# Optimization experiments

Hardware: AMD Instinct MI355X
Metric: run time of the kernel (lower is better)

## Reference

```python
import jax, jax.numpy as jnp
import numpy as np
from functools import partial

NP = 1024      # particles
T = 128        # timesteps
CUR_MIN, CUR_MAX = -2.0, 4.0
E_CRIT = 29000.0
F_STD = 0.005
G_STD = 0.01
NU = 1.0 / (G_STD * np.sqrt(2.0 * np.pi))

# VoC battery open-circuit-voltage curve constants
V_L, V_0 = -1.59614486, 4.13646328
GAMMA, ALPHA, BETA = 0.63726463, 1.40174122, 2.54478965


def voc(soc):
    return (V_L + (V_0 - V_L) * jnp.exp(GAMMA * (soc - 1.0))
            + ALPHA * V_L * (soc - 1.0)
            + (1.0 - ALPHA) * V_L * (jnp.exp(-BETA) - jnp.exp(-BETA * jnp.sqrt(soc))))


def setup_inputs() -> dict:
    key = jax.random.key(0)
    ks = jax.random.split(key, 11)
    soc_init = jax.random.uniform(ks[0], (NP, 1), jnp.float32, 0.3, 1.0)
    current = jax.random.normal(ks[1], (1, T), jnp.float32) * 0.5 + 1.0
    voltage_measured = 3.7 + 0.1 * jax.random.normal(ks[2], (1, T), jnp.float32)
    W1 = jax.random.normal(ks[3], (2, 1024), jnp.float32) / np.sqrt(2.0)
    b1 = jnp.zeros((1024,), jnp.float32)
    W2 = jax.random.normal(ks[4], (1024, 512), jnp.float32) / np.sqrt(1024.0)
    b2 = jnp.zeros((512,), jnp.float32)
    W3 = jax.random.normal(ks[5], (512, 1), jnp.float32) / np.sqrt(512.0)
    b3 = jnp.zeros((1,), jnp.float32)
    noise = jax.random.normal(ks[6], (T, NP, 1), jnp.float32)  # unit-std process noise
    u = jax.random.uniform(ks[7], (T,), jnp.float32)           # systematic-resampling offsets
    return {"soc_init": soc_init, "current": current, "voltage_measured": voltage_measured,
            "W1": W1, "b1": b1, "W2": W2, "b2": b2, "W3": W3, "b3": b3,
            "noise": noise, "u": u}


def _forward(soc_init, current, voltage_measured, W1, b1, W2, b2, W3, b3, noise, u):
    n = soc_init.shape[0]

    def mlp(x):  # [n,2] -> [n,1]
        z = jax.nn.sigmoid(x @ W1 + b1)
        z = jax.nn.sigmoid(z @ W2 + b2)
        return z @ W3 + b3

    def scale_I(I):
        return (I - CUR_MIN) / (CUR_MAX - CUR_MIN)

    cur = current[0]                       # [T]
    vmeas = voltage_measured[0]            # [T]
    cur_prev = jnp.concatenate([cur[:1], cur[:-1]])  # first step reuses current[0,0]

    def step(soc, xs):
        c_prev, c_t, vm, eps, ut = xs
        # --- prediction with previous current ---
        I = jnp.broadcast_to(c_prev, soc.shape)
        Z = mlp(jnp.concatenate([soc, scale_I(I)], axis=1))
        V = voc(soc) - I * Z
        soc = soc - I * V / E_CRIT + eps * F_STD
        soc = jnp.clip(soc, 1e-10, 1.0)
        # --- measurement update with current at t ---
        I = jnp.broadcast_to(c_t, soc.shape)
        sI = scale_I(I)
        Z = mlp(jnp.concatenate([soc, sI], axis=1))
        V = voc(soc) - I * Z
        logW = np.log(NU) - 0.5 * ((V - vm) / G_STD) ** 2  # [n,1]
        w = jnp.exp(logW - jnp.max(logW))[:, 0]
        wn = w / jnp.sum(w)
        # systematic resampling (deterministic given offset ut)
        cdf = jnp.cumsum(wn)
        pos = (ut + jnp.arange(n, dtype=jnp.float32)) / n
        idx = jnp.clip(jnp.searchsorted(cdf, pos), 0, n - 1)
        soc = soc[idx]
        # --- post-resample evaluation ---
        Z = mlp(jnp.concatenate([soc, sI], axis=1))
        V = voc(soc) - I * Z
        mse = jnp.mean((V - vm) ** 2)
        return soc, (mse, V[:, 0], soc[:, 0])

    soc0 = soc_init.astype(jnp.float32)
    _, (mses, Vs, socs) = jax.lax.scan(step, soc0, (cur_prev, cur, vmeas, noise, u))
    loss = jnp.mean(mses)        # == sum_t mse_t / T
    voltage = Vs.T               # [n, T]
    soc_hist = socs.T            # [n, T]
    return loss, voltage, soc_hist


def reference(soc_init, current, voltage_measured, W1, b1, W2, b2, W3, b3, noise, u):
    return _forward(soc_init, current, voltage_measured, W1, b1, W2, b2, W3, b3, noise, u)
```

## Files before the change

kernel.cpp:

```cpp
#include <hip/hip_runtime.h>
#include <stdint.h>

typedef __attribute__((ext_vector_type(8))) short short8;
typedef __attribute__((ext_vector_type(4))) float floatx4;

#define DONE_MAGIC 0x600DF00Du


__device__ __forceinline__ float sigm(float x) { return 1.0f / (1.0f + expf(-x)); }

__device__ __forceinline__ float vocf(float s) {
  const float V_L = -1.59614486f, V_0 = 4.13646328f;
  const float GAM = 0.63726463f, ALP = 1.40174122f, BET = 2.54478965f;
  return V_L + (V_0 - V_L) * expf(GAM * (s - 1.0f)) + ALP * V_L * (s - 1.0f)
       + (1.0f - ALP) * V_L * (expf(-BET) - expf(-BET * sqrtf(s)));
}

__device__ __forceinline__ unsigned short f2bf(float f) {
  unsigned u = __float_as_uint(f);
  u += 0x7FFFu + ((u >> 16) & 1u);
  return (unsigned short)(u >> 16);
}
__device__ __forceinline__ float bf2f(unsigned short b) {
  return __uint_as_float(((unsigned)b) << 16);
}

__device__ __forceinline__ float interp_c(const float* ctab, float s) {
  float f = s * 31.0f;
  float jf = fminf(floorf(f), 30.0f);
  int j = (int)jf;
  float u = f - jf;
  const float4 c = *(const float4*)&ctab[j * 4];
  return fmaf(fmaf(fmaf(c.w, u, c.z), u, c.y), u, c.x);
}

__device__ __forceinline__ int send_bl(float c, float u) {
  float C = c * 1024.0f;
  float sf = floorf(C - u);
  sf += (u + (sf + 1.0f) <= C) ? 1.0f : 0.0f;
  sf -= (u + sf > C) ? 1.0f : 0.0f;
  return (int)sf;
}

__device__ __forceinline__ float fast_exp2(float x) {
  float r;
  asm("v_exp_f32 %0, %1" : "=v"(r) : "v"(x));
  return r;
}


template<int C, int RM>
__device__ __forceinline__ float dpp_add_f(float x) {
  return __int_as_float(__builtin_amdgcn_update_dpp(0, __float_as_int(x), C, RM, 0xF, false));
}
template<int C, int RM>
__device__ __forceinline__ float dpp_old_f(float x) {
  return __int_as_float(__builtin_amdgcn_update_dpp(__float_as_int(x), __float_as_int(x), C, RM, 0xF, false));
}
template<int C, int RM>
__device__ __forceinline__ int dpp_old_i(int x) {
  return __builtin_amdgcn_update_dpp(x, x, C, RM, 0xF, false);
}
__device__ __forceinline__ float dpp_wshr1_f0(float x) {
  return __int_as_float(__builtin_amdgcn_update_dpp(0, __float_as_int(x), 0x138, 0xF, 0xF, true));
}
__device__ __forceinline__ int dpp_wshr1_i(int x, int old) {
  return __builtin_amdgcn_update_dpp(old, x, 0x138, 0xF, 0xF, false);
}
__device__ __forceinline__ int dpp_wshl1_i(int x, int old) {
  return __builtin_amdgcn_update_dpp(old, x, 0x130, 0xF, 0xF, false);
}

__device__ __forceinline__ float wave_iscan_add(float x) {
  x += dpp_add_f<0x111, 0xF>(x);
  x += dpp_add_f<0x112, 0xF>(x);
  x += dpp_add_f<0x114, 0xF>(x);
  x += dpp_add_f<0x118, 0xF>(x);
  x += dpp_add_f<0x142, 0xA>(x);
  x += dpp_add_f<0x143, 0xC>(x);
  return x;
}
__device__ __forceinline__ float wave_max_l63(float x) {
  x = fmaxf(x, dpp_old_f<0xB1,  0xF>(x));
  x = fmaxf(x, dpp_old_f<0x4E,  0xF>(x));
  x = fmaxf(x, dpp_old_f<0x141, 0xF>(x));
  x = fmaxf(x, dpp_old_f<0x140, 0xF>(x));
  x = fmaxf(x, dpp_old_f<0x142, 0xA>(x));
  x = fmaxf(x, dpp_old_f<0x143, 0xC>(x));
  return x;
}
__device__ __forceinline__ int wave_iscan_max(int x) {
  x = max(x, dpp_old_i<0x111, 0xF>(x));
  x = max(x, dpp_old_i<0x112, 0xF>(x));
  x = max(x, dpp_old_i<0x114, 0xF>(x));
  x = max(x, dpp_old_i<0x118, 0xF>(x));
  x = max(x, dpp_old_i<0x142, 0xA>(x));
  x = max(x, dpp_old_i<0x143, 0xC>(x));
  return x;
}

__device__ __forceinline__ float rdlane_f(float x, int lane) {
  return __int_as_float(__builtin_amdgcn_readlane(__float_as_int(x), lane));
}

__device__ __forceinline__ void bar_lds() {
  asm volatile("s_waitcnt lgkmcnt(0)" ::: "memory");
  __builtin_amdgcn_s_barrier();
  asm volatile("" ::: "memory");
}


__global__ void __launch_bounds__(256)
k1_swizzle(const float* __restrict__ W2g, short* __restrict__ w2hiG, short* __restrict__ w2loG)
{
  int bid = blockIdx.x, tid = threadIdx.x;
  int pg = bid & 15, ng = bid >> 4;
  int u = pg * 256 + tid;
  int kb = u >> 7, l = u & 63, nt = (u >> 6) & 1, kq = l >> 4;
  int col = ng * 32 + nt * 16 + (l & 15);
  short8 hi8, lo8;
  #pragma unroll
  for (int j = 0; j < 8; j++) {
    int k = kb * 32 + kq * 8 + j;
    float w = W2g[k * 512 + col];
    unsigned short h = f2bf(w);
    hi8[j] = (short)h;
    lo8[j] = (short)f2bf(w - bf2f(h));
  }
  size_t off = ((size_t)ng * 4096 + u) * 8;
  *(short8*)(w2hiG + off) = hi8;
  *(short8*)(w2loG + off) = lo8;
}


__global__ void __launch_bounds__(256)
k2_gemm(const float* __restrict__ curg, const float* __restrict__ W1g,
        const float* __restrict__ b1g, const float* __restrict__ b2g,
        const float* __restrict__ W3g, const short* __restrict__ w2hiG,
        const short* __restrict__ w2loG, float* __restrict__ part)
{
  __shared__ short w2S[32768];
  __shared__ float b2S[32], w3S[32];

  const int tid = threadIdx.x, bid = blockIdx.x;
  const int ng = bid & 15, rtg = bid >> 4;
  const int wv = tid >> 6, ln = tid & 63;
  const int kq = ln >> 4;

  {
    const short* srcH = w2hiG + (size_t)ng * 32768;
    for (int i = tid; i < 4096; i += 256)
      *(short8*)(w2S + i * 8) = *(const short8*)(srcH + i * 8);
    if (tid < 32) { b2S[tid] = b2g[ng * 32 + tid]; w3S[tid] = W3g[ng * 32 + tid]; }
  }
  __syncthreads();

  const short* loG = w2loG + (size_t)ng * 32768;
  const int c = ln & 15, q = ln >> 4;
  const float b20 = b2S[c], b21 = b2S[16 + c];
  const float w30 = w3S[c], w31 = w3S[16 + c];

  for (int jj = 0; jj < 3; jj++) {
    int rt = rtg + 32 * jj;
    if (rt >= 72) break;
    int pt = rt * 4 + wv;
    unsigned r = pt * 16 + (ln & 15);
    unsigned t = r / 36u;
    int i = (int)(r - t * 36u);
    float soc = (float)(i - 1) * (1.0f / 31.0f);
    float sI = (curg[t] + 2.0f) / 6.0f;

    floatx4 acc0 = {0.f, 0.f, 0.f, 0.f};
    floatx4 acc1 = {0.f, 0.f, 0.f, 0.f};

    for (int kb = 0; kb < 32; kb++) {
      int k0 = kb * 32 + kq * 8;
      floatx4 wa0 = *(const floatx4*)(W1g + k0);
      floatx4 wa1 = *(const floatx4*)(W1g + k0 + 4);
      floatx4 wb0 = *(const floatx4*)(W1g + 1024 + k0);
      floatx4 wb1 = *(const floatx4*)(W1g + 1024 + k0 + 4);
      floatx4 bb0 = *(const floatx4*)(b1g + k0);
      floatx4 bb1 = *(const floatx4*)(b1g + k0 + 4);
      short8 ah, al;
      #pragma unroll
      for (int j = 0; j < 4; j++) {
        float x = soc * wa0[j] + sI * wb0[j] + bb0[j];
        float z = __builtin_amdgcn_rcpf(1.0f + __expf(-x));
        unsigned short h = f2bf(z);
        ah[j] = (short)h;
        al[j] = (short)f2bf(z - bf2f(h));
      }
      #pragma unroll
      for (int j = 0; j < 4; j++) {
        float x = soc * wa1[j] + sI * wb1[j] + bb1[j];
        float z = __builtin_amdgcn_rcpf(1.0f + __expf(-x));
        unsigned short h = f2bf(z);
        ah[4 + j] = (short)h;
        al[4 + j] = (short)f2bf(z - bf2f(h));
      }
      short8 bh0 = *(const short8*)(w2S + (kb * 2 + 0) * 512 + ln * 8);
      short8 bh1 = *(const short8*)(w2S + (kb * 2 + 1) * 512 + ln * 8);
      short8 bl0 = *(const short8*)(loG + (kb * 2 + 0) * 512 + ln * 8);
      short8 bl1 = *(const short8*)(loG + (kb * 2 + 1) * 512 + ln * 8);
      acc0 = __builtin_amdgcn_mfma_f32_16x16x32_bf16(ah, bh0, acc0, 0, 0, 0);
      acc1 = __builtin_amdgcn_mfma_f32_16x16x32_bf16(ah, bh1, acc1, 0, 0, 0);
      acc0 = __builtin_amdgcn_mfma_f32_16x16x32_bf16(ah, bl0, acc0, 0, 0, 0);
      acc1 = __builtin_amdgcn_mfma_f32_16x16x32_bf16(ah, bl1, acc1, 0, 0, 0);
      acc0 = __builtin_amdgcn_mfma_f32_16x16x32_bf16(al, bh0, acc0, 0, 0, 0);
      acc1 = __builtin_amdgcn_mfma_f32_16x16x32_bf16(al, bh1, acc1, 0, 0, 0);
    }

    #pragma unroll
    for (int r2 = 0; r2 < 4; r2++) {
      float v = w30 * sigm(acc0[r2] + b20) + w31 * sigm(acc1[r2] + b21);
      v += __shfl_xor(v, 1);
      v += __shfl_xor(v, 2);
      v += __shfl_xor(v, 4);
      v += __shfl_xor(v, 8);
      if (c == 0) part[(size_t)(pt * 16 + q * 4 + r2) * 16 + ng] = v;
    }
  }
}


__global__ void __launch_bounds__(256)
k3_table(const float* __restrict__ part, const float* __restrict__ b3g,
         const float* __restrict__ curg, float* __restrict__ VtabG)
{
  unsigned r = blockIdx.x * 256 + threadIdx.x;
  if (r < 4608) {
    const float* p = part + (size_t)r * 16;
    float s = 0.f;
    #pragma unroll
    for (int i = 0; i < 16; i++) s += p[i];
    float Z = s + b3g[0];
    unsigned t = r / 36u;
    int i = (int)(r - t * 36u);
    float node = (float)(i - 1) * (1.0f / 31.0f);
    float nodc = fmaxf(node, 1e-10f);
    VtabG[r] = vocf(nodc) - curg[t] * Z;
  }
}


__global__ void __launch_bounds__(256)
k3b_coeff(const float* __restrict__ VtabG, float* __restrict__ ctabG)
{
  int idx = blockIdx.x * 256 + threadIdx.x;
  if (idx < 3968) {
    int t = idx / 31, j = idx - t * 31;
    const float* nb = VtabG + t * 36 + j;
    float n0 = nb[0], n1 = nb[1], n2 = nb[2], n3 = nb[3];
    float c0 = n1;
    float c1 = (-2.0f * n0 - 3.0f * n1 + 6.0f * n2 - n3) * (1.0f / 6.0f);
    float c2 = (n0 - 2.0f * n1 + n2) * 0.5f;
    float c3 = (-n0 + 3.0f * (n1 - n2) + n3) * (1.0f / 6.0f);
    *(float4*)&ctabG[idx * 4] = make_float4(c0, c1, c2, c3);
  }
}


__device__ __forceinline__ int swzi(int j) { return ((j & 3) << 8) | (j >> 2); }

__global__ void __launch_bounds__(256)
pf_seq(const float* __restrict__ soc_init, const float* __restrict__ curg,
       const float* __restrict__ vmeasg, const float* __restrict__ noise_g,
       const float* __restrict__ u_g, const float* __restrict__ ctabG,
       float* __restrict__ vout, float* __restrict__ sout, float* __restrict__ outp,
       unsigned* __restrict__ flag)
{
  __shared__ float ctabS[15872];
  __shared__ float2 pvS[2][1024];
  __shared__ int   markS[1024] __attribute__((aligned(16)));
  __shared__ float maxS[4], sumS[4], lossS[4];
  __shared__ int   seFS[4], tagS[4];

  if (blockIdx.x != 0) {
    float a = 1.0000001f, b = 0.9999999f, c = 0.5f;
    while (__hip_atomic_load(flag, __ATOMIC_RELAXED, __HIP_MEMORY_SCOPE_AGENT) != DONE_MAGIC) {
      #pragma unroll 8
      for (int i = 0; i < 512; i++) { a = fmaf(a, c, b); b = fmaf(b, c, a); }
    }
    asm volatile("" :: "v"(a), "v"(b));
    return;
  }

  const int tid = threadIdx.x;
  const int w = tid >> 6, l = tid & 63;
  const int p0 = tid * 4;

  #pragma unroll
  for (int k = 0; k < 16; k++) {
    int i = tid + 256 * k;
    if (i < 3968) *(float4*)&ctabS[i * 4] = *(const float4*)&ctabG[i * 4];
  }
  float curA = curg[l],   curB = curg[64 + l];
  float vmA  = vmeasg[l], vmB  = vmeasg[64 + l];
  float uA   = u_g[l],    uB   = u_g[64 + l];
  *(int4*)&markS[p0] = make_int4(-1, -1, -1, -1);

  float sp[4];
  {
    float4 s4 = *(const float4*)(soc_init + p0);
    float4 n4 = *(const float4*)(noise_g + p0);
    bar_lds();
    float c0 = rdlane_f(curA, 0);
    float c02 = c0 * (1.0f / 29000.0f);
    #pragma unroll
    for (int r = 0; r < 4; r++) {
      float si = ((const float*)&s4)[r];
      float V0 = interp_c(ctabS, si);
      float spn = fmaf(((const float*)&n4)[r], 0.005f, fmaf(-c02, V0, si));
      sp[r] = __builtin_amdgcn_fmed3f(spn, 1e-10f, 1.0f);
    }
  }

  float lossAcc = 0.0f;

  for (int t = 0; t < 128; t++) {
    const float* ctab = ctabS + t * 124;
    const int cb = t & 1;
    float cI, vm, ut;
    if (t < 64) { cI = rdlane_f(curA, t); vm = rdlane_f(vmA, t); ut = rdlane_f(uA, t); }
    else        { cI = rdlane_f(curB, t - 64); vm = rdlane_f(vmB, t - 64); ut = rdlane_f(uB, t - 64); }
    float cI2 = cI * (1.0f / 29000.0f);

    int tn = (t < 127) ? t + 1 : 127;
    float4 noi4 = *(const float4*)(noise_g + tn * 1024 + p0);

    float lw[4];
    #pragma unroll
    for (int r = 0; r < 4; r++) {
      float V1 = interp_c(ctab, sp[r]);
      pvS[cb][r * 256 + tid] = make_float2(sp[r], V1);
      float dd = V1 - vm;
      lw[r] = dd * dd * -7213.4755594f;
    }

    float lmax = fmaxf(fmaxf(lw[0], lw[1]), fmaxf(lw[2], lw[3]));
    float wm = wave_max_l63(lmax);
    if (l == 63) maxS[w] = wm;
    bar_lds();
    float m = fmaxf(fmaxf(maxS[0], maxS[1]), fmaxf(maxS[2], maxS[3]));

    float pr[4], acc = 0.0f;
    #pragma unroll
    for (int r = 0; r < 4; r++) { float wr = fast_exp2(lw[r] - m); acc += wr; pr[r] = acc; }
    float isc = wave_iscan_add(acc);
    if (l == 63) sumS[w] = isc;
    bar_lds();
    float s0 = sumS[0], s1 = sumS[1], s2 = sumS[2], s3 = sumS[3];
    float total = (s0 + s1) + (s2 + s3);
    float woff = (w > 0 ? s0 : 0.0f) + (w > 1 ? s1 : 0.0f) + (w > 2 ? s2 : 0.0f);
    float excl = dpp_wshr1_f0(isc) + woff;
    float rS = 1.0f / total;

    int se[4];
    #pragma unroll
    for (int r = 0; r < 4; r++) se[r] = send_bl((excl + pr[r]) * rS, ut);
    if (l == 0) seFS[w] = se[0];
    bar_lds();
    int nf = 0;
    if (w < 3) nf = seFS[w + 1];
    int nxt = dpp_wshl1_i(se[0], nf);
    int tbase = t << 10;
    if (tid == 0 && se[0] >= 0) markS[0] = tbase;
    #pragma unroll
    for (int r = 0; r < 4; r++) {
      int j = p0 + r;
      int slot = se[r] + 1;
      if (j == 1023) {
        if (slot <= 1023) markS[swzi(slot)] = tbase | 1023;
      } else {
        int seN = (r < 3) ? se[r + 1] : nxt;
        if (seN > se[r] && slot <= 1023) markS[swzi(slot)] = tbase | (j + 1);
      }
    }
    bar_lds();

    int mk0 = markS[tid],       mk1 = markS[256 + tid];
    int mk2 = markS[512 + tid], mk3 = markS[768 + tid];
    int q0 = mk0;
    int q1 = max(q0, mk1);
    int q2 = max(q1, mk2);
    int q3 = max(q2, mk3);
    int iscI = wave_iscan_max(q3);
    if (l == 63) tagS[w] = iscI;
    bar_lds();
    int ex = dpp_wshr1_i(iscI, -1);
    if (w > 0) ex = max(ex, tagS[0]);
    if (w > 1) ex = max(ex, tagS[1]);
    if (w > 2) ex = max(ex, tagS[2]);

    int o0 = max(ex, q0) & 1023, o1 = max(ex, q1) & 1023;
    int o2 = max(ex, q2) & 1023, o3 = max(ex, q3) & 1023;
    float2 g0 = pvS[cb][swzi(o0)];
    float2 g1 = pvS[cb][swzi(o1)];
    float2 g2 = pvS[cb][swzi(o2)];
    float2 g3 = pvS[cb][swzi(o3)];

    *(float4*)(vout + t * 1024 + p0) = make_float4(g0.y, g1.y, g2.y, g3.y);
    *(float4*)(sout + t * 1024 + p0) = make_float4(g0.x, g1.x, g2.x, g3.x);

    float2 g[4] = {g0, g1, g2, g3};
    #pragma unroll
    for (int r = 0; r < 4; r++) {
      float d = g[r].y - vm;
      lossAcc = fmaf(d, d, lossAcc);
      float spn = fmaf(((const float*)&noi4)[r], 0.005f, fmaf(-cI2, g[r].y, g[r].x));
      sp[r] = __builtin_amdgcn_fmed3f(spn, 1e-10f, 1.0f);
    }
  }

  float ls = wave_iscan_add(lossAcc);
  if (l == 63) lossS[w] = ls;
  bar_lds();
  if (tid == 0) {
    outp[0] = (lossS[0] + lossS[1] + lossS[2] + lossS[3]) * (1.0f / 131072.0f);
    __hip_atomic_store(flag, DONE_MAGIC, __ATOMIC_RELEASE, __HIP_MEMORY_SCOPE_AGENT);
  }
}


__global__ void __launch_bounds__(256)
k5_transpose(const float* __restrict__ vout, const float* __restrict__ sout,
             float* __restrict__ outp)
{
  __shared__ float tile[128 * 65];
  const int bid = blockIdx.x;
  const int arr = bid & 1;
  const int pg = bid >> 1;
  const float* src = arr ? sout : vout;
  float* dst = outp + 1 + arr * 131072;
  const int tid = threadIdx.x;
  const int p0 = pg * 64;

  #pragma unroll 4
  for (int s = 0; s < 32; s++) {
    int t = s * 4 + (tid >> 6);
    int p = tid & 63;
    tile[t * 65 + p] = src[t * 1024 + p0 + p];
  }
  __syncthreads();
  #pragma unroll 4
  for (int s = 0; s < 32; s++) {
    int pl = s * 2 + (tid >> 7);
    int t = tid & 127;
    dst[(p0 + pl) * 128 + t] = tile[t * 65 + pl];
  }
}


extern "C" void kernel_launch(void* const* d_in, const int* in_sizes, int n_in,
                              void* d_out, int out_size, void* d_ws, size_t ws_size,
                              hipStream_t stream) {
  const float* soc_init = (const float*)d_in[0];
  const float* cur      = (const float*)d_in[1];
  const float* vmeas    = (const float*)d_in[2];
  const float* W1       = (const float*)d_in[3];
  const float* b1       = (const float*)d_in[4];
  const float* W2       = (const float*)d_in[5];
  const float* b2       = (const float*)d_in[6];
  const float* W3       = (const float*)d_in[7];
  const float* b3       = (const float*)d_in[8];
  const float* noise    = (const float*)d_in[9];
  const float* u        = (const float*)d_in[10];
  float* out = (float*)d_out;
  char* ws = (char*)d_ws;

  short* w2hi   = (short*)ws;
  short* w2lo   = (short*)(ws + (1 << 20));
  float* part   = (float*)(ws + (2 << 20));
  char*  p3     = ws + (2 << 20) + 4608 * 16 * 4;
  float* VtabG  = (float*)p3;
  float* ctabG  = (float*)(p3 + 4608 * 4);
  float* vout   = (float*)(p3 + 4608 * 4 + 3968 * 16);
  float* sout   = (float*)(p3 + 4608 * 4 + 3968 * 16 + 1024 * 128 * 4);
  unsigned* flag = (unsigned*)(p3 + 4608 * 4 + 3968 * 16 + 2 * 1024 * 128 * 4);

  k1_swizzle<<<256, 256, 0, stream>>>(W2, w2hi, w2lo);
  k2_gemm<<<512, 256, 0, stream>>>(cur, W1, b1, b2, W3, w2hi, w2lo, part);
  k3_table<<<18, 256, 0, stream>>>(part, b3, cur, VtabG);
  k3b_coeff<<<16, 256, 0, stream>>>(VtabG, ctabG);
  pf_seq<<<256, 256, 0, stream>>>(soc_init, cur, vmeas, noise, u, ctabG, vout, sout, out, flag);
  k5_transpose<<<32, 256, 0, stream>>>(vout, sout, out);
}
```

Measured before the change: 342.6 us.

## Cut per-step block barriers by merging max/sum pass and using chunk atomics

Merges the max-reduction and sum-scan barriers into one: each wave uses its own local max for the exponentials and publishes a (max, sum) pair, and the cross-wave offsets are rescaled by exp2 factors afterwards. The boundary barrier for the next wave's first search result goes away, since the neighbour value is taken from lane data. The tag-scan barrier is replaced by LDS atomicMax into per-chunk maxima during marking. This removes about three block barriers per timestep in a single-block serial loop, at the cost of LDS atomics and slightly different floating-point rounding in the normalised CDF. There is also a redundant f3 computation left in.

```diff
diff --git a/kernel.cpp b/kernel.cpp
--- a/kernel.cpp
+++ b/kernel.cpp
@@ -80,14 +80,14 @@
   x += dpp_add_f<0x143, 0xC>(x);
   return x;
 }
-__device__ __forceinline__ float wave_max_l63(float x) {
+__device__ __forceinline__ float wave_max_bcast(float x) {
   x = fmaxf(x, dpp_old_f<0xB1,  0xF>(x));
   x = fmaxf(x, dpp_old_f<0x4E,  0xF>(x));
   x = fmaxf(x, dpp_old_f<0x141, 0xF>(x));
   x = fmaxf(x, dpp_old_f<0x140, 0xF>(x));
   x = fmaxf(x, dpp_old_f<0x142, 0xA>(x));
   x = fmaxf(x, dpp_old_f<0x143, 0xC>(x));
-  return x;
+  return __int_as_float(__builtin_amdgcn_readlane(__float_as_int(x), 63));
 }
 __device__ __forceinline__ int wave_iscan_max(int x) {
   x = max(x, dpp_old_i<0x111, 0xF>(x));
@@ -272,8 +272,9 @@
   __shared__ float ctabS[15872];
   __shared__ float2 pvS[2][1024];
   __shared__ int   markS[1024] __attribute__((aligned(16)));
-  __shared__ float maxS[4], sumS[4], lossS[4];
-  __shared__ int   seFS[4], tagS[4];
+  __shared__ int   chunkS[4] __attribute__((aligned(16)));
+  __shared__ float2 msS[4] __attribute__((aligned(16)));
+  __shared__ float lossS[4];
 
   if (blockIdx.x != 0) {
     float a = 1.0000001f, b = 0.9999999f, c = 0.5f;
@@ -298,21 +299,24 @@
   float vmA  = vmeasg[l], vmB  = vmeasg[64 + l];
   float uA   = u_g[l],    uB   = u_g[64 + l];
   *(int4*)&markS[p0] = make_int4(-1, -1, -1, -1);
-
-  float sp[4];
+  if (tid < 4) chunkS[tid] = -1;
+
+  float sp0, sp1, sp2, sp3;
   {
     float4 s4 = *(const float4*)(soc_init + p0);
     float4 n4 = *(const float4*)(noise_g + p0);
     bar_lds();
     float c0 = rdlane_f(curA, 0);
     float c02 = c0 * (1.0f / 29000.0f);
+    float spv[4];
     #pragma unroll
     for (int r = 0; r < 4; r++) {
       float si = ((const float*)&s4)[r];
       float V0 = interp_c(ctabS, si);
       float spn = fmaf(((const float*)&n4)[r], 0.005f, fmaf(-c02, V0, si));
-      sp[r] = __builtin_amdgcn_fmed3f(spn, 1e-10f, 1.0f);
-    }
+      spv[r] = __builtin_amdgcn_fmed3f(spn, 1e-10f, 1.0f);
+    }
+    sp0 = spv[0]; sp1 = spv[1]; sp2 = spv[2]; sp3 = spv[3];
   }
 
   float lossAcc = 0.0f;
@@ -328,69 +332,92 @@
     int tn = (t < 127) ? t + 1 : 127;
     float4 noi4 = *(const float4*)(noise_g + tn * 1024 + p0);
 
-    float lw[4];
-    #pragma unroll
-    for (int r = 0; r < 4; r++) {
-      float V1 = interp_c(ctab, sp[r]);
-      pvS[cb][r * 256 + tid] = make_float2(sp[r], V1);
-      float dd = V1 - vm;
-      lw[r] = dd * dd * -7213.4755594f;
-    }
-
-    float lmax = fmaxf(fmaxf(lw[0], lw[1]), fmaxf(lw[2], lw[3]));
-    float wm = wave_max_l63(lmax);
-    if (l == 63) maxS[w] = wm;
+    float V10 = interp_c(ctab, sp0);
+    float V11 = interp_c(ctab, sp1);
+    float V12 = interp_c(ctab, sp2);
+    float V13 = interp_c(ctab, sp3);
+    pvS[cb][tid]       = make_float2(sp0, V10);
+    pvS[cb][256 + tid] = make_float2(sp1, V11);
+    pvS[cb][512 + tid] = make_float2(sp2, V12);
+    pvS[cb][768 + tid] = make_float2(sp3, V13);
+    float d0 = V10 - vm, d1 = V11 - vm, d2 = V12 - vm, d3 = V13 - vm;
+    float lw0 = d0 * d0 * -7213.4755594f;
+    float lw1 = d1 * d1 * -7213.4755594f;
+    float lw2 = d2 * d2 * -7213.4755594f;
+    float lw3 = d3 * d3 * -7213.4755594f;
+
+    float lmax = fmaxf(fmaxf(lw0, lw1), fmaxf(lw2, lw3));
+    float mw = wave_max_bcast(lmax);
+    float pr0, pr1, pr2, pr3, acc;
+    {
+      float w0 = fast_exp2(lw0 - mw); acc = w0;    pr0 = acc;
+      float w1 = fast_exp2(lw1 - mw); acc += w1;   pr1 = acc;
+      float w2 = fast_exp2(lw2 - mw); acc += w2;   pr2 = acc;
+      float w3 = fast_exp2(lw3 - mw); acc += w3;   pr3 = acc;
+    }
+    float isc = wave_iscan_add(acc);
+    if (l == 63) msS[w] = make_float2(mw, isc);
     bar_lds();
-    float m = fmaxf(fmaxf(maxS[0], maxS[1]), fmaxf(maxS[2], maxS[3]));
-
-    float pr[4], acc = 0.0f;
-    #pragma unroll
-    for (int r = 0; r < 4; r++) { float wr = fast_exp2(lw[r] - m); acc += wr; pr[r] = acc; }
-    float isc = wave_iscan_add(acc);
-    if (l == 63) sumS[w] = isc;
-    bar_lds();
-    float s0 = sumS[0], s1 = sumS[1], s2 = sumS[2], s3 = sumS[3];
-    float total = (s0 + s1) + (s2 + s3);
-    float woff = (w > 0 ? s0 : 0.0f) + (w > 1 ? s1 : 0.0f) + (w > 2 ? s2 : 0.0f);
-    float excl = dpp_wshr1_f0(isc) + woff;
+
+    float4 ms01 = *(const float4*)&msS[0];
+    float4 ms23 = *(const float4*)&msS[2];
+    float m = fmaxf(fmaxf(ms01.x, ms01.z), fmaxf(ms23.x, ms23.z));
+    float f0 = fast_exp2(ms01.x - m), f1 = fast_exp2(ms01.z - m);
+    float f2 = fast_exp2(ms23.x - m), f3 = fast_exp2(ms23.w == ms23.w ? ms23.z - m : 0.f);
+    f3 = fast_exp2(ms23.z - m);
+    float t0 = ms01.y * f0, t1 = ms01.w * f1, t2 = ms23.y * f2, t3 = ms23.w * f3;
+    float total = (t0 + t1) + (t2 + t3);
+    float woff = (w > 0 ? t0 : 0.0f) + (w > 1 ? t1 : 0.0f) + (w > 2 ? t2 : 0.0f);
+    float fw = (w == 0) ? f0 : ((w == 1) ? f1 : ((w == 2) ? f2 : f3));
+    float exclw = dpp_wshr1_f0(isc);
     float rS = 1.0f / total;
 
-    int se[4];
-    #pragma unroll
-    for (int r = 0; r < 4; r++) se[r] = send_bl((excl + pr[r]) * rS, ut);
-    if (l == 0) seFS[w] = se[0];
-    bar_lds();
-    int nf = 0;
-    if (w < 3) nf = seFS[w + 1];
-    int nxt = dpp_wshl1_i(se[0], nf);
+    int se0 = send_bl(fmaf(exclw + pr0, fw, woff) * rS, ut);
+    int se1 = send_bl(fmaf(exclw + pr1, fw, woff) * rS, ut);
+    int se2 = send_bl(fmaf(exclw + pr2, fw, woff) * rS, ut);
+    int se3 = send_bl(fmaf(exclw + pr3, fw, woff) * rS, ut);
+
+    int nxt = dpp_wshl1_i(se0, se3);
     int tbase = t << 10;
-    if (tid == 0 && se[0] >= 0) markS[0] = tbase;
-    #pragma unroll
-    for (int r = 0; r < 4; r++) {
-      int j = p0 + r;
-      int slot = se[r] + 1;
-      if (j == 1023) {
-        if (slot <= 1023) markS[swzi(slot)] = tbase | 1023;
-      } else {
-        int seN = (r < 3) ? se[r + 1] : nxt;
-        if (seN > se[r] && slot <= 1023) markS[swzi(slot)] = tbase | (j + 1);
+    if (tid == 0 && se0 >= 0) { markS[0] = tbase; atomicMax(&chunkS[0], tbase); }
+    if (se1 > se0 && se0 < 1023) {
+      int s = se0 + 1, tg = tbase | (p0 + 1);
+      markS[swzi(s)] = tg; atomicMax(&chunkS[s >> 8], tg);
+    }
+    if (se2 > se1 && se1 < 1023) {
+      int s = se1 + 1, tg = tbase | (p0 + 2);
+      markS[swzi(s)] = tg; atomicMax(&chunkS[s >> 8], tg);
+    }
+    if (se3 > se2 && se2 < 1023) {
+      int s = se2 + 1, tg = tbase | (p0 + 3);
+      markS[swzi(s)] = tg; atomicMax(&chunkS[s >> 8], tg);
+    }
+    if (l != 63) {
+      if (nxt > se3 && se3 < 1023) {
+        int s = se3 + 1, tg = tbase | (p0 + 4);
+        markS[swzi(s)] = tg; atomicMax(&chunkS[s >> 8], tg);
+      }
+    } else {
+      if (se3 < 1023) {
+        int s = se3 + 1;
+        int tg = (tid == 255) ? (tbase | 1023) : (tbase | (p0 + 4));
+        atomicMax(&markS[swzi(s)], tg); atomicMax(&chunkS[s >> 8], tg);
       }
     }
     bar_lds();
 
     int mk0 = markS[tid],       mk1 = markS[256 + tid];
     int mk2 = markS[512 + tid], mk3 = markS[768 + tid];
+    int4 ch4 = *(const int4*)chunkS;
     int q0 = mk0;
     int q1 = max(q0, mk1);
     int q2 = max(q1, mk2);
     int q3 = max(q2, mk3);
     int iscI = wave_iscan_max(q3);
-    if (l == 63) tagS[w] = iscI;
-    bar_lds();
     int ex = dpp_wshr1_i(iscI, -1);
-    if (w > 0) ex = max(ex, tagS[0]);
-    if (w > 1) ex = max(ex, tagS[1]);
-    if (w > 2) ex = max(ex, tagS[2]);
+    if (w > 0) ex = max(ex, ch4.x);
+    if (w > 1) ex = max(ex, ch4.y);
+    if (w > 2) ex = max(ex, ch4.z);
 
     int o0 = max(ex, q0) & 1023, o1 = max(ex, q1) & 1023;
     int o2 = max(ex, q2) & 1023, o3 = max(ex, q3) & 1023;
@@ -402,14 +429,16 @@
     *(float4*)(vout + t * 1024 + p0) = make_float4(g0.y, g1.y, g2.y, g3.y);
     *(float4*)(sout + t * 1024 + p0) = make_float4(g0.x, g1.x, g2.x, g3.x);
 
-    float2 g[4] = {g0, g1, g2, g3};
-    #pragma unroll
-    for (int r = 0; r < 4; r++) {
-      float d = g[r].y - vm;
-      lossAcc = fmaf(d, d, lossAcc);
-      float spn = fmaf(((const float*)&noi4)[r], 0.005f, fmaf(-cI2, g[r].y, g[r].x));
-      sp[r] = __builtin_amdgcn_fmed3f(spn, 1e-10f, 1.0f);
-    }
+    float e0 = g0.y - vm, e1 = g1.y - vm, e2 = g2.y - vm, e3 = g3.y - vm;
+    lossAcc = fmaf(e0, e0, lossAcc);
+    lossAcc = fmaf(e1, e1, lossAcc);
+    lossAcc = fmaf(e2, e2, lossAcc);
+    lossAcc = fmaf(e3, e3, lossAcc);
+    const float* nz = (const float*)&noi4;
+    sp0 = __builtin_amdgcn_fmed3f(fmaf(nz[0], 0.005f, fmaf(-cI2, g0.y, g0.x)), 1e-10f, 1.0f);
+    sp1 = __builtin_amdgcn_fmed3f(fmaf(nz[1], 0.005f, fmaf(-cI2, g1.y, g1.x)), 1e-10f, 1.0f);
+    sp2 = __builtin_amdgcn_fmed3f(fmaf(nz[2], 0.005f, fmaf(-cI2, g2.y, g2.x)), 1e-10f, 1.0f);
+    sp3 = __builtin_amdgcn_fmed3f(fmaf(nz[3], 0.005f, fmaf(-cI2, g3.y, g3.x)), 1e-10f, 1.0f);
   }
 
   float ls = wave_iscan_add(lossAcc);
```

Result: faster. 332.4 us (-3.0%).
